# Kernel tuning notes

Measured on AMD Instinct MI355X. Metric: run time of the kernel, lower is better.

## Reference

```python
import jax, jax.numpy as jnp
import numpy as np

N = 100000
IN_C = 256
OUT_C = 256
E = 500000


def gcn_conv(x, W, b, edges):
    """PyG GCNConv: add self-loops, symmetric D^-1/2 (A+I) D^-1/2 normalization,
    then scatter-add of transformed source features into targets, plus bias."""
    n = x.shape[0]
    loop = jnp.arange(n, dtype=edges.dtype)
    row = jnp.concatenate([edges[0], loop])  # source
    col = jnp.concatenate([edges[1], loop])  # target
    deg = jax.ops.segment_sum(jnp.ones_like(col, dtype=x.dtype), col, num_segments=n)
    dis = jax.lax.rsqrt(deg)  # deg >= 1 after self-loops
    norm = dis[row] * dis[col]  # [E+n]
    h = x @ W  # [n, out]
    msg = h[row] * norm[:, None]  # gather + scale
    return jax.ops.segment_sum(msg, col, num_segments=n) + b


def setup_inputs() -> dict:
    key = jax.random.key(0)
    ks = jax.random.split(key, 24)
    x = jax.random.normal(ks[0], (N, IN_C), dtype=jnp.float32)
    edges00 = jax.random.randint(ks[1], (2, E), 0, N, dtype=jnp.int32)
    edges01 = jax.random.randint(ks[2], (2, E), 0, N, dtype=jnp.int32)
    edges10 = jax.random.randint(ks[3], (2, E), 0, N, dtype=jnp.int32)
    edges11 = jax.random.randint(ks[4], (2, E), 0, N, dtype=jnp.int32)
    t0 = (jax.random.uniform(ks[5], (N,)) > 0.5).astype(jnp.float32)
    t1 = 1.0 - t0
    scale = 1.0 / np.sqrt(IN_C)
    W1 = jax.random.normal(ks[6], (IN_C, OUT_C), dtype=jnp.float32) * scale
    W2 = jax.random.normal(ks[7], (IN_C, OUT_C), dtype=jnp.float32) * scale
    W3 = jax.random.normal(ks[8], (IN_C, OUT_C), dtype=jnp.float32) * scale
    W4 = jax.random.normal(ks[9], (IN_C, OUT_C), dtype=jnp.float32) * scale
    b1 = jnp.zeros((OUT_C,), jnp.float32)
    b2 = jnp.zeros((OUT_C,), jnp.float32)
    b3 = jnp.zeros((OUT_C,), jnp.float32)
    b4 = jnp.zeros((OUT_C,), jnp.float32)
    p0 = jax.random.normal(ks[10], (OUT_C,), dtype=jnp.float32)
    p1 = jax.random.normal(ks[11], (OUT_C,), dtype=jnp.float32)
    p2 = jax.random.normal(ks[12], (OUT_C,), dtype=jnp.float32)
    p3 = jax.random.normal(ks[13], (OUT_C,), dtype=jnp.float32)
    p4 = jax.random.normal(ks[14], (OUT_C,), dtype=jnp.float32)
    p5 = jax.random.normal(ks[15], (OUT_C,), dtype=jnp.float32)
    return dict(x=x, edges00=edges00, edges01=edges01, edges10=edges10, edges11=edges11,
                type0_idx=t0, type1_idx=t1,
                W1=W1, b1=b1, W2=W2, b2=b2, W3=W3, b3=b3, W4=W4, b4=b4,
                p0=p0, p1=p1, p2=p2, p3=p3, p4=p4, p5=p5)


def reference(x, edges00, edges01, edges10, edges11, type0_idx, type1_idx,
              W1, b1, W2, b2, W3, b3, W4, b4, p0, p1, p2, p3, p4, p5):
    # x0/x1: first feature column masked by node type, broadcast over out channels
    x0c = type0_idx * x[:, 0]  # [N]
    x1c = type1_idx * x[:, 0]
    x00 = gcn_conv(x, W1, b1, edges00)
    x01 = gcn_conv(x, W2, b2, edges01)
    x10 = gcn_conv(x, W3, b3, edges10)
    x11 = gcn_conv(x, W4, b4, edges11)
    out = (x0c[:, None] * p0 + x1c[:, None] * p1
           + x00 * p2 + x01 * p3 + x10 * p4 + x11 * p5)
    return out
```

## Files before the change

### kernel.cpp

```cpp
#include <hip/hip_runtime.h>


typedef __bf16 v8bf __attribute__((ext_vector_type(8)));
typedef float v4f __attribute__((ext_vector_type(4)));

__device__ __forceinline__ unsigned short f2bf(float f) {
  unsigned u = __float_as_uint(f);
  u += 0x7fffu + ((u >> 16) & 1u);
  return (unsigned short)(u >> 16);
}
__device__ __forceinline__ float bf2f(unsigned short s) {
  return __uint_as_float(((unsigned)s) << 16);
}
__device__ __forceinline__ void async_ld16(const void* g, void* l) {
  __builtin_amdgcn_global_load_lds((__attribute__((address_space(1))) void*)g,
                                   (__attribute__((address_space(3))) void*)l,
                                   16, 0, 0);
}

__global__ void lc_zero(int* __restrict__ p, int n) {
  int i = blockIdx.x * 256 + threadIdx.x;
  if (i < n) p[i] = 0;
}

__global__ void lc_hist(const int* __restrict__ e0, const int* __restrict__ e1,
                        const int* __restrict__ e2, const int* __restrict__ e3,
                        int* __restrict__ hist, int N, int E) {
  int e = blockIdx.x * 256 + threadIdx.x;
  if (e >= E) return;
  int k = blockIdx.y;
  const int* ed = (k == 0) ? e0 : (k == 1) ? e1 : (k == 2) ? e2 : e3;
  int col = ed[E + e];
  atomicAdd(&hist[k * N + col], 1);
}

__global__ void lc_dis(const int* __restrict__ hist, float* __restrict__ dis, int M) {
  int i = blockIdx.x * 256 + threadIdx.x;
  if (i < M) dis[i] = rsqrtf((float)(hist[i] + 1));
}

__global__ void lc_scan1(const int* __restrict__ in, int* __restrict__ outp,
                         int* __restrict__ bsum, int M) {
  __shared__ int tmp[256];
  int t = threadIdx.x, i = blockIdx.x * 256 + t;
  int v = (i < M) ? in[i] : 0;
  tmp[t] = v;
  __syncthreads();
  for (int off = 1; off < 256; off <<= 1) {
    int add = (t >= off) ? tmp[t - off] : 0;
    __syncthreads();
    tmp[t] += add;
    __syncthreads();
  }
  if (i < M) outp[i] = tmp[t] - v;
  if (t == 255) bsum[blockIdx.x] = tmp[255];
}

__global__ void lc_scan2(int* __restrict__ bsum, int nb) {
  __shared__ int tmp[256];
  __shared__ int carry_s;
  int t = threadIdx.x;
  if (t == 0) carry_s = 0;
  __syncthreads();
  for (int base = 0; base < nb; base += 256) {
    int i = base + t;
    int v = (i < nb) ? bsum[i] : 0;
    tmp[t] = v;
    __syncthreads();
    for (int off = 1; off < 256; off <<= 1) {
      int add = (t >= off) ? tmp[t - off] : 0;
      __syncthreads();
      tmp[t] += add;
      __syncthreads();
    }
    int carry = carry_s;
    int total = tmp[255];
    if (i < nb) bsum[i] = carry + tmp[t] - v;
    __syncthreads();
    if (t == 0) carry_s = carry + total;
    __syncthreads();
  }
}

__global__ void lc_scan3(int* __restrict__ rp, int* __restrict__ cursor,
                         const int* __restrict__ bsum, int M) {
  int i = blockIdx.x * 256 + threadIdx.x;
  if (i < M) {
    int v = rp[i] + bsum[blockIdx.x];
    rp[i] = v;
    cursor[i] = v;
  }
}

__global__ void lc_fill(const int* __restrict__ e0, const int* __restrict__ e1,
                        const int* __restrict__ e2, const int* __restrict__ e3,
                        int* __restrict__ cursor, const float* __restrict__ dis,
                        int2* __restrict__ payload, int N, int E) {
  int e = blockIdx.x * 256 + threadIdx.x;
  if (e >= E) return;
  int k = blockIdx.y;
  const int* ed = (k == 0) ? e0 : (k == 1) ? e1 : (k == 2) ? e2 : e3;
  int src = ed[e], col = ed[E + e];
  int pos = atomicAdd(&cursor[k * N + col], 1);
  float nrm = dis[k * N + src] * dis[k * N + col];
  payload[pos] = make_int2(src, __float_as_int(nrm));
}

__global__ void lc_bias(const float* __restrict__ b1, const float* __restrict__ b2,
                        const float* __restrict__ b3, const float* __restrict__ b4,
                        const float* __restrict__ p2, const float* __restrict__ p3,
                        const float* __restrict__ p4, const float* __restrict__ p5,
                        float* __restrict__ biasc) {
  int c = threadIdx.x;
  biasc[c] = b1[c] * p2[c] + b2[c] * p3[c] + b3[c] * p4[c] + b4[c] * p5[c];
}

__global__ void lc_prep(const float* __restrict__ W1, const float* __restrict__ W2,
                        const float* __restrict__ W3, const float* __restrict__ W4,
                        const float* __restrict__ p2, const float* __restrict__ p3,
                        const float* __restrict__ p4, const float* __restrict__ p5,
                        unsigned short* __restrict__ Wt) {
  int b = blockIdx.x;
  int k = b >> 8, co = b & 255;
  int kk = threadIdx.x;
  const float* W = (k == 0) ? W1 : (k == 1) ? W2 : (k == 2) ? W3 : W4;
  const float* p = (k == 0) ? p2 : (k == 1) ? p3 : (k == 2) ? p4 : p5;
  Wt[(size_t)co * 1024 + k * 256 + kk] = f2bf(W[kk * 256 + co] * p[co]);
}

__global__ void lc_cvt(const float4* __restrict__ x4, ushort4* __restrict__ xb4,
                       const float* __restrict__ t0, const float* __restrict__ t1,
                       float* __restrict__ m0, float* __restrict__ m1, int n4) {
  int i = blockIdx.x * 256 + threadIdx.x;
  if (i >= n4) return;
  float4 v = x4[i];
  ushort4 r;
  r.x = f2bf(v.x); r.y = f2bf(v.y); r.z = f2bf(v.z); r.w = f2bf(v.w);
  xb4[i] = r;
  if ((i & 63) == 0) {
    int n = i >> 6;
    float xc = v.x;
    m0[n] = t0[n] * xc;
    m1[n] = t1[n] * xc;
  }
}

__global__ __launch_bounds__(256) void lc_aggx(
    const unsigned short* __restrict__ xb, unsigned short* __restrict__ Agg,
    int aggw, int kcount, int kbase, const int* __restrict__ rp,
    const int* __restrict__ hist, const float* __restrict__ dis,
    const int2* __restrict__ payload, int N) {
  int t = threadIdx.x;
  int w = t >> 6, lane = t & 63;
  int n, k, koff;
  if (kcount == 4) { n = blockIdx.x; k = w; koff = k * 256; }
  else { n = blockIdx.x * 4 + w; k = kbase; koff = 0; }
  if (n >= N) return;
  int c = lane * 4;
  int idx = k * N + n;

  float dn = dis[idx];
  float s = dn * dn;
  ushort4 hv = *(const ushort4*)&xb[(size_t)n * 256 + c];
  float a0 = bf2f(hv.x) * s, a1 = bf2f(hv.y) * s;
  float a2 = bf2f(hv.z) * s, a3 = bf2f(hv.w) * s;

  int start = rp[idx];
  int cnt = hist[idx];
  int i = 0;
  for (; i + 4 <= cnt; i += 4) {
    int2 e0 = payload[start + i];
    int2 e1 = payload[start + i + 1];
    int2 e2 = payload[start + i + 2];
    int2 e3 = payload[start + i + 3];
    ushort4 g0 = *(const ushort4*)&xb[(size_t)e0.x * 256 + c];
    ushort4 g1 = *(const ushort4*)&xb[(size_t)e1.x * 256 + c];
    ushort4 g2 = *(const ushort4*)&xb[(size_t)e2.x * 256 + c];
    ushort4 g3 = *(const ushort4*)&xb[(size_t)e3.x * 256 + c];
    float n0 = __int_as_float(e0.y), n1 = __int_as_float(e1.y);
    float n2 = __int_as_float(e2.y), n3 = __int_as_float(e3.y);
    a0 += bf2f(g0.x) * n0 + bf2f(g1.x) * n1 + bf2f(g2.x) * n2 + bf2f(g3.x) * n3;
    a1 += bf2f(g0.y) * n0 + bf2f(g1.y) * n1 + bf2f(g2.y) * n2 + bf2f(g3.y) * n3;
    a2 += bf2f(g0.z) * n0 + bf2f(g1.z) * n1 + bf2f(g2.z) * n2 + bf2f(g3.z) * n3;
    a3 += bf2f(g0.w) * n0 + bf2f(g1.w) * n1 + bf2f(g2.w) * n2 + bf2f(g3.w) * n3;
  }
  for (; i < cnt; i++) {
    int2 e0 = payload[start + i];
    ushort4 g0 = *(const ushort4*)&xb[(size_t)e0.x * 256 + c];
    float n0 = __int_as_float(e0.y);
    a0 += bf2f(g0.x) * n0;
    a1 += bf2f(g0.y) * n0;
    a2 += bf2f(g0.z) * n0;
    a3 += bf2f(g0.w) * n0;
  }
  ushort4 r;
  r.x = f2bf(a0); r.y = f2bf(a1); r.z = f2bf(a2); r.w = f2bf(a3);
  *(ushort4*)&Agg[(size_t)n * aggw + koff + c] = r;
}

__global__ __launch_bounds__(256) void lc_gemm(
    const unsigned short* __restrict__ A, int strideA,
    const unsigned short* __restrict__ B, int strideB, int K,
    float* __restrict__ out, int Mrows, int addprev, int doepi,
    const float* __restrict__ m0, const float* __restrict__ m1,
    const float* __restrict__ p0, const float* __restrict__ p1,
    const float* __restrict__ biasc) {
  __shared__ alignas(16) unsigned short As[128 * 32];
  __shared__ alignas(16) unsigned short Bs[128 * 32];
  int t = threadIdx.x;
  int w = t >> 6, lane = t & 63;
  int wm = w & 1, wn = w >> 1;
  int quad = lane >> 4, l16 = lane & 15;
  int row0 = blockIdx.x * 128, col0 = blockIdx.y * 128;

  v4f acc[4][4];
#pragma unroll
  for (int mt = 0; mt < 4; mt++)
#pragma unroll
    for (int nt = 0; nt < 4; nt++) {
      v4f z = {0.f, 0.f, 0.f, 0.f};
      acc[mt][nt] = z;
    }

  for (int kk = 0; kk < K; kk += 32) {
#pragma unroll
    for (int p = 0; p < 2; p++) {
      int cbase = p * 256 + w * 64;
      int cA = cbase + lane;
      int rl = cA >> 2, c16 = cA & 3;
      int grow = row0 + rl;
      if (grow >= Mrows) grow = Mrows - 1;
      async_ld16(A + (size_t)grow * strideA + kk + c16 * 8, &As[cbase * 8]);
      async_ld16(B + (size_t)(col0 + rl) * strideB + kk + c16 * 8, &Bs[cbase * 8]);
    }
    __syncthreads();

    v8bf af[4], bfr[4];
#pragma unroll
    for (int mt = 0; mt < 4; mt++) {
      int r = wm * 64 + mt * 16 + l16;
      af[mt] = *(const v8bf*)&As[r * 32 + quad * 8];
    }
#pragma unroll
    for (int nt = 0; nt < 4; nt++) {
      int n = wn * 64 + nt * 16 + l16;
      bfr[nt] = *(const v8bf*)&Bs[n * 32 + quad * 8];
    }
#pragma unroll
    for (int mt = 0; mt < 4; mt++)
#pragma unroll
      for (int nt = 0; nt < 4; nt++)
        acc[mt][nt] =
            __builtin_amdgcn_mfma_f32_16x16x32_bf16(af[mt], bfr[nt], acc[mt][nt], 0, 0, 0);
    __syncthreads();
  }

  float pc0[4], pc1[4], bc[4];
#pragma unroll
  for (int nt = 0; nt < 4; nt++) {
    int gcol = col0 + wn * 64 + nt * 16 + l16;
    pc0[nt] = doepi ? p0[gcol] : 0.f;
    pc1[nt] = doepi ? p1[gcol] : 0.f;
    bc[nt] = doepi ? biasc[gcol] : 0.f;
  }
#pragma unroll
  for (int mt = 0; mt < 4; mt++)
#pragma unroll
    for (int r = 0; r < 4; r++) {
      int grow = row0 + wm * 64 + mt * 16 + quad * 4 + r;
      if (grow >= Mrows) continue;
      float m0v = 0.f, m1v = 0.f;
      if (doepi) { m0v = m0[grow]; m1v = m1[grow]; }
#pragma unroll
      for (int nt = 0; nt < 4; nt++) {
        int gcol = col0 + wn * 64 + nt * 16 + l16;
        size_t o = (size_t)grow * 256 + gcol;
        float v = acc[mt][nt][r];
        if (addprev) v += out[o];
        if (doepi) v += m0v * pc0[nt] + m1v * pc1[nt] + bc[nt];
        out[o] = v;
      }
    }
}

extern "C" void kernel_launch(void* const* d_in, const int* in_sizes, int n_in,
                              void* d_out, int out_size, void* d_ws, size_t ws_size,
                              hipStream_t stream) {
  const float* x = (const float*)d_in[0];
  const int* e00 = (const int*)d_in[1];
  const int* e01 = (const int*)d_in[2];
  const int* e10 = (const int*)d_in[3];
  const int* e11 = (const int*)d_in[4];
  const float* t0 = (const float*)d_in[5];
  const float* t1 = (const float*)d_in[6];
  const float* W1 = (const float*)d_in[7];
  const float* b1 = (const float*)d_in[8];
  const float* W2 = (const float*)d_in[9];
  const float* b2 = (const float*)d_in[10];
  const float* W3 = (const float*)d_in[11];
  const float* b3 = (const float*)d_in[12];
  const float* W4 = (const float*)d_in[13];
  const float* b4 = (const float*)d_in[14];
  const float* p0 = (const float*)d_in[15];
  const float* p1 = (const float*)d_in[16];
  const float* p2 = (const float*)d_in[17];
  const float* p3 = (const float*)d_in[18];
  const float* p4 = (const float*)d_in[19];
  const float* p5 = (const float*)d_in[20];
  float* out = (float*)d_out;

  int N = in_sizes[0] / 256;
  int E = in_sizes[1] / 2;
  int M4 = 4 * N;
  int nb = (M4 + 255) / 256;

  char* wp = (char*)d_ws;
  auto carve = [&](size_t bytes) {
    void* r = (void*)wp;
    wp += (bytes + 255) & ~(size_t)255;
    return r;
  };
  unsigned short* xb = (unsigned short*)carve((size_t)N * 256 * 2);
  unsigned short* Wt = (unsigned short*)carve((size_t)256 * 1024 * 2);
  int* hist = (int*)carve((size_t)M4 * 4);
  float* dis = (float*)carve((size_t)M4 * 4);
  int* rp = (int*)carve((size_t)M4 * 4);
  int* cursor = (int*)carve((size_t)M4 * 4);
  int* bsum = (int*)carve((size_t)nb * 4);
  float* biasc = (float*)carve(256 * 4);
  float* m0 = (float*)carve((size_t)N * 4);
  float* m1 = (float*)carve((size_t)N * 4);
  int2* payload = (int2*)carve((size_t)4 * E * 8);
  size_t used = (size_t)(wp - (char*)d_ws);
  size_t remain = (ws_size > used) ? ws_size - used : 0;
  bool fat = remain >= (size_t)N * 1024 * 2;
  unsigned short* Agg = (unsigned short*)wp;

  int gE = (E + 255) / 256;
  int gM = (M4 + 255) / 256;

  lc_zero<<<gM, 256, 0, stream>>>(hist, M4);
  lc_hist<<<dim3(gE, 4), 256, 0, stream>>>(e00, e01, e10, e11, hist, N, E);
  lc_dis<<<gM, 256, 0, stream>>>(hist, dis, M4);
  lc_scan1<<<nb, 256, 0, stream>>>(hist, rp, bsum, M4);
  lc_scan2<<<1, 256, 0, stream>>>(bsum, nb);
  lc_scan3<<<nb, 256, 0, stream>>>(rp, cursor, bsum, M4);
  lc_fill<<<dim3(gE, 4), 256, 0, stream>>>(e00, e01, e10, e11, cursor, dis, payload, N, E);
  lc_bias<<<1, 256, 0, stream>>>(b1, b2, b3, b4, p2, p3, p4, p5, biasc);
  lc_prep<<<1024, 256, 0, stream>>>(W1, W2, W3, W4, p2, p3, p4, p5, Wt);
  lc_cvt<<<(N * 64 + 255) / 256, 256, 0, stream>>>((const float4*)x, (ushort4*)xb,
                                                   t0, t1, m0, m1, N * 64);

  int gemm_mb = (N + 127) / 128;
  if (fat) {
    lc_aggx<<<N, 256, 0, stream>>>(xb, Agg, 1024, 4, 0, rp, hist, dis, payload, N);
    lc_gemm<<<dim3(gemm_mb, 2), 256, 0, stream>>>(Agg, 1024, Wt, 1024, 1024, out, N,
                                                  0, 1, m0, m1, p0, p1, biasc);
  } else {
    for (int k = 0; k < 4; k++) {
      lc_aggx<<<(N + 3) / 4, 256, 0, stream>>>(xb, Agg, 256, 1, k, rp, hist, dis,
                                               payload, N);
      lc_gemm<<<dim3(gemm_mb, 2), 256, 0, stream>>>(Agg, 256, Wt + k * 256, 1024, 256,
                                                    out, N, (k > 0) ? 1 : 0,
                                                    (k == 3) ? 1 : 0, m0, m1, p0, p1,
                                                    biasc);
    }
  }
}
```

Baseline: 720.6 us.

## Widen GEMM tile to full output width, prefetch payload, drop cursor atomics

Several independent changes. The CSR fill now writes each edge to its row start plus a rank recorded by the histogram atomic, so the second pass of atomics and the cursor array go away. The dis computation is folded into the first scan kernel. The aggregation kernel software-prefetches the next batch of payload entries with nontemporal loads and stores its result nontemporally. The GEMM now covers all 256 output columns per block, so the A tile is loaded once instead of twice, at the cost of double the accumulator registers and B shared memory, which may lower occupancy.

```diff
diff --git a/kernel.cpp b/kernel.cpp
--- a/kernel.cpp
+++ b/kernel.cpp
@@ -25,25 +25,21 @@
 
 __global__ void lc_hist(const int* __restrict__ e0, const int* __restrict__ e1,
                         const int* __restrict__ e2, const int* __restrict__ e3,
-                        int* __restrict__ hist, int N, int E) {
+                        int* __restrict__ hist, int* __restrict__ rnk, int N, int E) {
   int e = blockIdx.x * 256 + threadIdx.x;
   if (e >= E) return;
   int k = blockIdx.y;
   const int* ed = (k == 0) ? e0 : (k == 1) ? e1 : (k == 2) ? e2 : e3;
   int col = ed[E + e];
-  atomicAdd(&hist[k * N + col], 1);
-}
-
-__global__ void lc_dis(const int* __restrict__ hist, float* __restrict__ dis, int M) {
-  int i = blockIdx.x * 256 + threadIdx.x;
-  if (i < M) dis[i] = rsqrtf((float)(hist[i] + 1));
+  rnk[(size_t)k * E + e] = atomicAdd(&hist[k * N + col], 1);
 }
 
 __global__ void lc_scan1(const int* __restrict__ in, int* __restrict__ outp,
-                         int* __restrict__ bsum, int M) {
+                         int* __restrict__ bsum, float* __restrict__ dis, int M) {
   __shared__ int tmp[256];
   int t = threadIdx.x, i = blockIdx.x * 256 + t;
   int v = (i < M) ? in[i] : 0;
+  if (i < M) dis[i] = rsqrtf((float)(v + 1));
   tmp[t] = v;
   __syncthreads();
   for (int off = 1; off < 256; off <<= 1) {
@@ -82,26 +78,22 @@
   }
 }
 
-__global__ void lc_scan3(int* __restrict__ rp, int* __restrict__ cursor,
-                         const int* __restrict__ bsum, int M) {
+__global__ void lc_scan3(int* __restrict__ rp, const int* __restrict__ bsum, int M) {
   int i = blockIdx.x * 256 + threadIdx.x;
-  if (i < M) {
-    int v = rp[i] + bsum[blockIdx.x];
-    rp[i] = v;
-    cursor[i] = v;
-  }
+  if (i < M) rp[i] += bsum[blockIdx.x];
 }
 
 __global__ void lc_fill(const int* __restrict__ e0, const int* __restrict__ e1,
                         const int* __restrict__ e2, const int* __restrict__ e3,
-                        int* __restrict__ cursor, const float* __restrict__ dis,
-                        int2* __restrict__ payload, int N, int E) {
+                        const int* __restrict__ rp, const int* __restrict__ rnk,
+                        const float* __restrict__ dis, int2* __restrict__ payload,
+                        int N, int E) {
   int e = blockIdx.x * 256 + threadIdx.x;
   if (e >= E) return;
   int k = blockIdx.y;
   const int* ed = (k == 0) ? e0 : (k == 1) ? e1 : (k == 2) ? e2 : e3;
   int src = ed[e], col = ed[E + e];
-  int pos = atomicAdd(&cursor[k * N + col], 1);
+  int pos = rp[k * N + col] + rnk[(size_t)k * E + e];
   float nrm = dis[k * N + src] * dis[k * N + col];
   payload[pos] = make_int2(src, __float_as_int(nrm));
 }
@@ -149,7 +141,7 @@
     const unsigned short* __restrict__ xb, unsigned short* __restrict__ Agg,
     int aggw, int kcount, int kbase, const int* __restrict__ rp,
     const int* __restrict__ hist, const float* __restrict__ dis,
-    const int2* __restrict__ payload, int N) {
+    const long long* __restrict__ payload, int N) {
   int t = threadIdx.x;
   int w = t >> 6, lane = t & 63;
   int n, k, koff;
@@ -167,35 +159,49 @@
 
   int start = rp[idx];
   int cnt = hist[idx];
-  int i = 0;
-  for (; i + 4 <= cnt; i += 4) {
-    int2 e0 = payload[start + i];
-    int2 e1 = payload[start + i + 1];
-    int2 e2 = payload[start + i + 2];
-    int2 e3 = payload[start + i + 3];
-    ushort4 g0 = *(const ushort4*)&xb[(size_t)e0.x * 256 + c];
-    ushort4 g1 = *(const ushort4*)&xb[(size_t)e1.x * 256 + c];
-    ushort4 g2 = *(const ushort4*)&xb[(size_t)e2.x * 256 + c];
-    ushort4 g3 = *(const ushort4*)&xb[(size_t)e3.x * 256 + c];
-    float n0 = __int_as_float(e0.y), n1 = __int_as_float(e1.y);
-    float n2 = __int_as_float(e2.y), n3 = __int_as_float(e3.y);
-    a0 += bf2f(g0.x) * n0 + bf2f(g1.x) * n1 + bf2f(g2.x) * n2 + bf2f(g3.x) * n3;
-    a1 += bf2f(g0.y) * n0 + bf2f(g1.y) * n1 + bf2f(g2.y) * n2 + bf2f(g3.y) * n3;
-    a2 += bf2f(g0.z) * n0 + bf2f(g1.z) * n1 + bf2f(g2.z) * n2 + bf2f(g3.z) * n3;
-    a3 += bf2f(g0.w) * n0 + bf2f(g1.w) * n1 + bf2f(g2.w) * n2 + bf2f(g3.w) * n3;
-  }
-  for (; i < cnt; i++) {
-    int2 e0 = payload[start + i];
-    ushort4 g0 = *(const ushort4*)&xb[(size_t)e0.x * 256 + c];
-    float n0 = __int_as_float(e0.y);
-    a0 += bf2f(g0.x) * n0;
-    a1 += bf2f(g0.y) * n0;
-    a2 += bf2f(g0.z) * n0;
-    a3 += bf2f(g0.w) * n0;
+  int nb4 = cnt >> 2;
+  long long pv0, pv1, pv2, pv3;
+  if (nb4 > 0) {
+    const long long* pp = payload + start;
+    pv0 = __builtin_nontemporal_load(pp);
+    pv1 = __builtin_nontemporal_load(pp + 1);
+    pv2 = __builtin_nontemporal_load(pp + 2);
+    pv3 = __builtin_nontemporal_load(pp + 3);
+    for (int b = 0; b < nb4; b++) {
+      int s0 = (int)pv0, s1 = (int)pv1, s2 = (int)pv2, s3 = (int)pv3;
+      float n0 = __int_as_float((int)(pv0 >> 32));
+      float n1 = __int_as_float((int)(pv1 >> 32));
+      float n2 = __int_as_float((int)(pv2 >> 32));
+      float n3 = __int_as_float((int)(pv3 >> 32));
+      ushort4 g0 = *(const ushort4*)&xb[(size_t)s0 * 256 + c];
+      ushort4 g1 = *(const ushort4*)&xb[(size_t)s1 * 256 + c];
+      ushort4 g2 = *(const ushort4*)&xb[(size_t)s2 * 256 + c];
+      ushort4 g3 = *(const ushort4*)&xb[(size_t)s3 * 256 + c];
+      if (b + 1 < nb4) {
+        const long long* pn = payload + start + (b + 1) * 4;
+        pv0 = __builtin_nontemporal_load(pn);
+        pv1 = __builtin_nontemporal_load(pn + 1);
+        pv2 = __builtin_nontemporal_load(pn + 2);
+        pv3 = __builtin_nontemporal_load(pn + 3);
+      }
+      a0 += bf2f(g0.x) * n0 + bf2f(g1.x) * n1 + bf2f(g2.x) * n2 + bf2f(g3.x) * n3;
+      a1 += bf2f(g0.y) * n0 + bf2f(g1.y) * n1 + bf2f(g2.y) * n2 + bf2f(g3.y) * n3;
+      a2 += bf2f(g0.z) * n0 + bf2f(g1.z) * n1 + bf2f(g2.z) * n2 + bf2f(g3.z) * n3;
+      a3 += bf2f(g0.w) * n0 + bf2f(g1.w) * n1 + bf2f(g2.w) * n2 + bf2f(g3.w) * n3;
+    }
+  }
+  for (int i = nb4 << 2; i < cnt; i++) {
+    long long pv = __builtin_nontemporal_load(payload + start + i);
+    int src = (int)pv;
+    float nr = __int_as_float((int)(pv >> 32));
+    ushort4 g = *(const ushort4*)&xb[(size_t)src * 256 + c];
+    a0 += bf2f(g.x) * nr; a1 += bf2f(g.y) * nr;
+    a2 += bf2f(g.z) * nr; a3 += bf2f(g.w) * nr;
   }
   ushort4 r;
   r.x = f2bf(a0); r.y = f2bf(a1); r.z = f2bf(a2); r.w = f2bf(a3);
-  *(ushort4*)&Agg[(size_t)n * aggw + koff + c] = r;
+  __builtin_nontemporal_store(*(const long long*)&r,
+                              (long long*)&Agg[(size_t)n * aggw + koff + c]);
 }
 
 __global__ __launch_bounds__(256) void lc_gemm(
@@ -206,18 +212,18 @@
     const float* __restrict__ p0, const float* __restrict__ p1,
     const float* __restrict__ biasc) {
   __shared__ alignas(16) unsigned short As[128 * 32];
-  __shared__ alignas(16) unsigned short Bs[128 * 32];
+  __shared__ alignas(16) unsigned short Bs[256 * 32];
   int t = threadIdx.x;
   int w = t >> 6, lane = t & 63;
   int wm = w & 1, wn = w >> 1;
   int quad = lane >> 4, l16 = lane & 15;
-  int row0 = blockIdx.x * 128, col0 = blockIdx.y * 128;
-
-  v4f acc[4][4];
+  int row0 = blockIdx.x * 128;
+
+  v4f acc[4][8];
 #pragma unroll
   for (int mt = 0; mt < 4; mt++)
 #pragma unroll
-    for (int nt = 0; nt < 4; nt++) {
+    for (int nt = 0; nt < 8; nt++) {
       v4f z = {0.f, 0.f, 0.f, 0.f};
       acc[mt][nt] = z;
     }
@@ -231,34 +237,38 @@
       int grow = row0 + rl;
       if (grow >= Mrows) grow = Mrows - 1;
       async_ld16(A + (size_t)grow * strideA + kk + c16 * 8, &As[cbase * 8]);
-      async_ld16(B + (size_t)(col0 + rl) * strideB + kk + c16 * 8, &Bs[cbase * 8]);
-    }
-    __syncthreads();
-
-    v8bf af[4], bfr[4];
+    }
+#pragma unroll
+    for (int p = 0; p < 4; p++) {
+      int cbase = p * 256 + w * 64;
+      int cB = cbase + lane;
+      int rl = cB >> 2, c16 = cB & 3;
+      async_ld16(B + (size_t)rl * strideB + kk + c16 * 8, &Bs[cbase * 8]);
+    }
+    __syncthreads();
+
+    v8bf af[4];
 #pragma unroll
     for (int mt = 0; mt < 4; mt++) {
       int r = wm * 64 + mt * 16 + l16;
       af[mt] = *(const v8bf*)&As[r * 32 + quad * 8];
     }
 #pragma unroll
-    for (int nt = 0; nt < 4; nt++) {
-      int n = wn * 64 + nt * 16 + l16;
-      bfr[nt] = *(const v8bf*)&Bs[n * 32 + quad * 8];
-    }
-#pragma unroll
-    for (int mt = 0; mt < 4; mt++)
-#pragma unroll
-      for (int nt = 0; nt < 4; nt++)
+    for (int nt = 0; nt < 8; nt++) {
+      int nr = wn * 128 + nt * 16 + l16;
+      v8bf bfr = *(const v8bf*)&Bs[nr * 32 + quad * 8];
+#pragma unroll
+      for (int mt = 0; mt < 4; mt++)
         acc[mt][nt] =
-            __builtin_amdgcn_mfma_f32_16x16x32_bf16(af[mt], bfr[nt], acc[mt][nt], 0, 0, 0);
-    __syncthreads();
-  }
-
-  float pc0[4], pc1[4], bc[4];
-#pragma unroll
-  for (int nt = 0; nt < 4; nt++) {
-    int gcol = col0 + wn * 64 + nt * 16 + l16;
+            __builtin_amdgcn_mfma_f32_16x16x32_bf16(af[mt], bfr, acc[mt][nt], 0, 0, 0);
+    }
+    __syncthreads();
+  }
+
+  float pc0[8], pc1[8], bc[8];
+#pragma unroll
+  for (int nt = 0; nt < 8; nt++) {
+    int gcol = wn * 128 + nt * 16 + l16;
     pc0[nt] = doepi ? p0[gcol] : 0.f;
     pc1[nt] = doepi ? p1[gcol] : 0.f;
     bc[nt] = doepi ? biasc[gcol] : 0.f;
@@ -272,8 +282,8 @@
       float m0v = 0.f, m1v = 0.f;
       if (doepi) { m0v = m0[grow]; m1v = m1[grow]; }
 #pragma unroll
-      for (int nt = 0; nt < 4; nt++) {
-        int gcol = col0 + wn * 64 + nt * 16 + l16;
+      for (int nt = 0; nt < 8; nt++) {
+        int gcol = wn * 128 + nt * 16 + l16;
         size_t o = (size_t)grow * 256 + gcol;
         float v = acc[mt][nt][r];
         if (addprev) v += out[o];
@@ -325,7 +335,7 @@
   int* hist = (int*)carve((size_t)M4 * 4);
   float* dis = (float*)carve((size_t)M4 * 4);
   int* rp = (int*)carve((size_t)M4 * 4);
-  int* cursor = (int*)carve((size_t)M4 * 4);
+  int* rnk = (int*)carve((size_t)4 * E * 4);
   int* bsum = (int*)carve((size_t)nb * 4);
   float* biasc = (float*)carve(256 * 4);
   float* m0 = (float*)carve((size_t)N * 4);
@@ -340,12 +350,12 @@
   int gM = (M4 + 255) / 256;
 
   lc_zero<<<gM, 256, 0, stream>>>(hist, M4);
-  lc_hist<<<dim3(gE, 4), 256, 0, stream>>>(e00, e01, e10, e11, hist, N, E);
-  lc_dis<<<gM, 256, 0, stream>>>(hist, dis, M4);
-  lc_scan1<<<nb, 256, 0, stream>>>(hist, rp, bsum, M4);
+  lc_hist<<<dim3(gE, 4), 256, 0, stream>>>(e00, e01, e10, e11, hist, rnk, N, E);
+  lc_scan1<<<nb, 256, 0, stream>>>(hist, rp, bsum, dis, M4);
   lc_scan2<<<1, 256, 0, stream>>>(bsum, nb);
-  lc_scan3<<<nb, 256, 0, stream>>>(rp, cursor, bsum, M4);
-  lc_fill<<<dim3(gE, 4), 256, 0, stream>>>(e00, e01, e10, e11, cursor, dis, payload, N, E);
+  lc_scan3<<<nb, 256, 0, stream>>>(rp, bsum, M4);
+  lc_fill<<<dim3(gE, 4), 256, 0, stream>>>(e00, e01, e10, e11, rp, rnk, dis,
+                                           payload, N, E);
   lc_bias<<<1, 256, 0, stream>>>(b1, b2, b3, b4, p2, p3, p4, p5, biasc);
   lc_prep<<<1024, 256, 0, stream>>>(W1, W2, W3, W4, p2, p3, p4, p5, Wt);
   lc_cvt<<<(N * 64 + 255) / 256, 256, 0, stream>>>((const float4*)x, (ushort4*)xb,
@@ -353,17 +363,17 @@
 
   int gemm_mb = (N + 127) / 128;
   if (fat) {
-    lc_aggx<<<N, 256, 0, stream>>>(xb, Agg, 1024, 4, 0, rp, hist, dis, payload, N);
-    lc_gemm<<<dim3(gemm_mb, 2), 256, 0, stream>>>(Agg, 1024, Wt, 1024, 1024, out, N,
-                                                  0, 1, m0, m1, p0, p1, biasc);
+    lc_aggx<<<N, 256, 0, stream>>>(xb, Agg, 1024, 4, 0, rp, hist, dis,
+                                   (const long long*)payload, N);
+    lc_gemm<<<gemm_mb, 256, 0, stream>>>(Agg, 1024, Wt, 1024, 1024, out, N, 0, 1,
+                                         m0, m1, p0, p1, biasc);
   } else {
     for (int k = 0; k < 4; k++) {
       lc_aggx<<<(N + 3) / 4, 256, 0, stream>>>(xb, Agg, 256, 1, k, rp, hist, dis,
-                                               payload, N);
-      lc_gemm<<<dim3(gemm_mb, 2), 256, 0, stream>>>(Agg, 256, Wt + k * 256, 1024, 256,
-                                                    out, N, (k > 0) ? 1 : 0,
-                                                    (k == 3) ? 1 : 0, m0, m1, p0, p1,
-                                                    biasc);
-    }
-  }
-}
+                                               (const long long*)payload, N);
+      lc_gemm<<<gemm_mb, 256, 0, stream>>>(Agg, 256, Wt + k * 256, 1024, 256, out, N,
+                                           (k > 0) ? 1 : 0, (k == 3) ? 1 : 0, m0, m1,
+                                           p0, p1, biasc);
+    }
+  }
+}
```

Result: slower. 805.3 us (+11.7%).
